# Optimization experiments

Hardware: AMD Instinct MI355X
Metric: run time of the kernel (lower is better)

## Reference

```python
import jax, jax.numpy as jnp
import numpy as np

B, C, H, W = 8, 128, 64, 64
INTER = C // 2

def setup_inputs() -> dict:
    key = jax.random.key(0)
    ks = jax.random.split(key, 9)
    s = 0.05
    return {
        "x": jax.random.normal(ks[0], (B, C, H, W), dtype=jnp.float32),
        "theta_w": jax.random.normal(ks[1], (INTER, C), dtype=jnp.float32) * s,
        "theta_b": jax.random.normal(ks[2], (INTER,), dtype=jnp.float32) * s,
        "phi_w": jax.random.normal(ks[3], (INTER, C), dtype=jnp.float32) * s,
        "phi_b": jax.random.normal(ks[4], (INTER,), dtype=jnp.float32) * s,
        "g_w": jax.random.normal(ks[5], (INTER, C), dtype=jnp.float32) * s,
        "g_b": jax.random.normal(ks[6], (INTER,), dtype=jnp.float32) * s,
        "out_w": jax.random.normal(ks[7], (C, INTER), dtype=jnp.float32) * s,
        "out_b": jax.random.normal(ks[8], (C,), dtype=jnp.float32) * s,
    }

def reference(x, theta_w, theta_b, phi_w, phi_b, g_w, g_b, out_w, out_b):
    b, c, h, w = x.shape
    xf = x.reshape(b, c, h * w)                                   # [b, C, n]
    # 1x1 convs == per-pixel channel matmuls
    theta = jnp.einsum('oc,bcn->bno', theta_w, xf) + theta_b       # [b, n, inter]
    phi = jnp.einsum('oc,bcn->bon', phi_w, xf) + phi_b[:, None]    # [b, inter, n]
    g = jnp.einsum('oc,bcn->bno', g_w, xf) + g_b                   # [b, n, inter]
    attn = jax.nn.softmax(jnp.einsum('bno,bom->bnm', theta, phi), axis=-1)  # [b, n, n]
    y = jnp.einsum('bnm,bmo->bon', attn, g)                        # [b, inter, n]
    out = jnp.einsum('oc,bcn->bon', out_w, y) + out_b[:, None]     # [b, C, n]
    return out.reshape(b, c, h, w) + x
```

## Files before the change

### kernel.cpp

```cpp
#include <hip/hip_runtime.h>
#include <hip/hip_bf16.h>
#include <cstdint>
#include <cmath>

#define N_PIX 4096
#define CH    128
#define DD    64
#define NBATCH 8
#define NT    32

typedef unsigned short u16;
typedef __attribute__((ext_vector_type(8))) short bf8_t;
typedef __attribute__((ext_vector_type(4))) float f4_t;
typedef __attribute__((ext_vector_type(16))) float f16v;
typedef uint32_t u32x4 __attribute__((ext_vector_type(4)));
typedef uint32_t u32x2 __attribute__((ext_vector_type(2)));

#define L2E 1.44269504088896340736f

#if __has_builtin(__builtin_amdgcn_exp2f)
  #define EXP2(x) __builtin_amdgcn_exp2f(x)
#else
  #define EXP2(x) exp2f(x)
#endif

__device__ __forceinline__ u16 f2b(float f) {
  union { float f; uint32_t u; } v; v.f = f;
  uint32_t u = v.u;
  return (u16)((u + 0x7fffu + ((u >> 16) & 1u)) >> 16);
}
__device__ __forceinline__ float b2f(u16 h) {
  union { uint32_t u; float f; } v; v.u = ((uint32_t)h) << 16;
  return v.f;
}
__device__ __forceinline__ uint32_t pack2(float a, float b) {
  return (uint32_t)f2b(a) | ((uint32_t)f2b(b) << 16);
}
__device__ __forceinline__ uint32_t pack2hw(float a, float b) {
  u16 lo = __builtin_bit_cast(u16, __float2bfloat16(a));
  u16 hi = __builtin_bit_cast(u16, __float2bfloat16(b));
  return (uint32_t)lo | ((uint32_t)hi << 16);
}
__device__ __forceinline__ f4_t mfma16(bf8_t a, bf8_t b, f4_t c) {
  return __builtin_amdgcn_mfma_f32_16x16x32_bf16(a, b, c, 0, 0, 0);
}
__device__ __forceinline__ f16v mfma32(bf8_t a, bf8_t b, f16v c) {
  return __builtin_amdgcn_mfma_f32_32x32x16_bf16(a, b, c, 0, 0, 0);
}
__device__ __forceinline__ void pl32swap(uint32_t &a, uint32_t &b) {
  u32x2 r = __builtin_amdgcn_permlane32_swap(a, b, false, false);
  a = r[0];
  b = r[1];
}

__global__ __launch_bounds__(256) void proj_kernel(
    const float* __restrict__ x,
    const float* __restrict__ tw, const float* __restrict__ tb,
    const float* __restrict__ pw, const float* __restrict__ pb,
    const float* __restrict__ gw, const float* __restrict__ gb,
    u16* __restrict__ theta_h, u16* __restrict__ phi_h, u16* __restrict__ gt_h) {
  __shared__ __align__(16) u16 xT[64][136];
  const int blk = blockIdx.x;
  const int b  = blk >> 6;
  const int n0 = (blk & 63) << 6;
  const int tid = threadIdx.x;

  #pragma unroll
  for (int i = 0; i < 8; ++i) {
    int idx = tid + i * 256;
    int px = (idx & 15) * 4;
    int c  = idx >> 4;
    float4 v = *(const float4*)(x + ((size_t)b * CH + c) * N_PIX + n0 + px);
    xT[px + 0][c] = f2b(v.x);
    xT[px + 1][c] = f2b(v.y);
    xT[px + 2][c] = f2b(v.z);
    xT[px + 3][c] = f2b(v.w);
  }
  __syncthreads();

  const int lane = tid & 63;
  const int w    = tid >> 6;
  const int l4   = lane >> 4, l15 = lane & 15;

  bf8_t bw[3][4];
  float bias[3];
  #pragma unroll
  for (int nt = 0; nt < 3; ++nt) {
    int op = 16 * (3 * w + nt) + l15;
    const float* wrow; float bv; float scl;
    if (op < 64)       { wrow = tw + op * CH;          bv = tb[op];        scl = L2E; }
    else if (op < 128) { wrow = pw + (op - 64) * CH;   bv = pb[op - 64];   scl = 1.f; }
    else               { wrow = gw + (op - 128) * CH;  bv = gb[op - 128];  scl = 1.f; }
    bias[nt] = bv * scl;
    #pragma unroll
    for (int ks = 0; ks < 4; ++ks) {
      const float* p = wrow + 32 * ks + l4 * 8;
      bf8_t v;
      #pragma unroll
      for (int j = 0; j < 8; ++j) v[j] = (short)f2b(p[j] * scl);
      bw[nt][ks] = v;
    }
  }

  f4_t acc[4][3];
  #pragma unroll
  for (int mt = 0; mt < 4; ++mt)
    #pragma unroll
    for (int nt = 0; nt < 3; ++nt) acc[mt][nt] = (f4_t){0.f, 0.f, 0.f, 0.f};

  #pragma unroll
  for (int mt = 0; mt < 4; ++mt) {
    #pragma unroll
    for (int ks = 0; ks < 4; ++ks) {
      bf8_t a = *(const bf8_t*)&xT[l15 + 16 * mt][32 * ks + l4 * 8];
      #pragma unroll
      for (int nt = 0; nt < 3; ++nt)
        acc[mt][nt] = mfma16(a, bw[nt][ks], acc[mt][nt]);
    }
  }

  #pragma unroll
  for (int nt = 0; nt < 3; ++nt) {
    int op = 16 * (3 * w + nt) + l15;
    #pragma unroll
    for (int mt = 0; mt < 4; ++mt) {
      #pragma unroll
      for (int r = 0; r < 4; ++r) {
        int q = n0 + 16 * mt + l4 * 4 + r;
        u16 h = f2b(acc[mt][nt][r] + bias[nt]);
        if (op < 64)       theta_h[((size_t)b * N_PIX + q) * DD + op] = h;
        else if (op < 128) phi_h[((size_t)b * N_PIX + q) * DD + (op - 64)] = h;
        else               gt_h[((size_t)b * DD + (op - 128)) * N_PIX + q] = h;
      }
    }
  }
}

__global__ __launch_bounds__(512, 4) void attn_kernel(
    const u16* __restrict__ theta_h, const u16* __restrict__ phi_h,
    const u16* __restrict__ gt_h, u16* __restrict__ y_h) {
  __shared__ __align__(16) u16 smem[32768];

  const int bid = blockIdx.x;
  const int lb  = (bid & 7) * 64 + (bid >> 3);
  const int b   = lb >> 6;
  const int q0  = (lb & 63) << 6;
  const int tid = threadIdx.x;
  const int l   = tid & 63;
  const int w   = tid >> 6;
  const int qg  = w & 1;
  const int mh  = w >> 1;
  const int l31 = l & 31;
  const int hi  = l >> 5;

  bf8_t th[4];
  {
    const u16* trow = theta_h + ((size_t)b * N_PIX + q0 + 32 * qg + l31) * DD;
    #pragma unroll
    for (int kk = 0; kk < 4; ++kk)
      th[kk] = *(const bf8_t*)(trow + 16 * kk + 8 * hi);
  }

  f16v yacc[2];
  #pragma unroll
  for (int ot = 0; ot < 2; ++ot)
    #pragma unroll
    for (int r = 0; r < 16; ++r) yacc[ot][r] = 0.f;
  float m_ = -1e30f, l_ = 0.f;

  const int pr  = tid >> 3, pc = tid & 7;
  const int go  = tid >> 4, gc = tid & 15;
  const u16* phA = phi_h + ((size_t)b * N_PIX + pr) * DD + pc * 8;
  const u16* gtA = gt_h + ((size_t)b * DD + go) * N_PIX + gc * 8;
  const int pO0 = pr * 64 + ((pc ^ (pr & 7)) << 3);
  const int pO1 = pO0 + 4096;
  const int gO0 = 8192 + go * 128 + ((gc ^ (go & 7)) << 3);
  const int gO1 = gO0 + 4096;

  uint4 v0, v1, v2, v3;
  #define LOADS(kb_) do {                                              \
    v0 = *(const uint4*)(phA + (size_t)(kb_) * 8192);                  \
    v1 = *(const uint4*)(phA + (size_t)(kb_) * 8192 + 4096);           \
    v2 = *(const uint4*)(gtA + (size_t)(kb_) * 128);                   \
    v3 = *(const uint4*)(gtA + (size_t)(kb_) * 128 + 32 * (size_t)N_PIX); \
  } while (0)
  #define WRITES(buf_) do {                                            \
    u16* base_ = smem + (buf_) * 16384;                                \
    *(uint4*)(base_ + pO0) = v0;                                       \
    *(uint4*)(base_ + pO1) = v1;                                       \
    *(uint4*)(base_ + gO0) = v2;                                       \
    *(uint4*)(base_ + gO1) = v3;                                       \
  } while (0)

  LOADS(0); WRITES(0);
  __syncthreads();

  const int prow  = 32 * mh + l31;
  const int pbase = prow * 64;
  const int pkey  = prow & 7;

  for (int t = 0; t < NT; ++t) {
    const int cur = t & 1;
    if (t < NT - 1) LOADS(t + 1);
    const u16* pb = smem + cur * 16384;
    const u16* gb = pb + 8192;

    f16v st;
    #pragma unroll
    for (int r = 0; r < 16; ++r) st[r] = 0.f;
    #pragma unroll
    for (int kk = 0; kk < 4; ++kk) {
      bf8_t a = *(const bf8_t*)(pb + pbase + (((2 * kk + hi) ^ pkey) << 3));
      st = mfma32(a, th[kk], st);
    }

    float x0 = fmaxf(st[0], st[1]),   x1 = fmaxf(st[2], st[3]);
    float x2 = fmaxf(st[4], st[5]),   x3 = fmaxf(st[6], st[7]);
    float x4 = fmaxf(st[8], st[9]),   x5 = fmaxf(st[10], st[11]);
    float x6 = fmaxf(st[12], st[13]), x7 = fmaxf(st[14], st[15]);
    float y0 = fmaxf(fmaxf(x0, x1), fmaxf(x2, x3));
    float y1 = fmaxf(fmaxf(x4, x5), fmaxf(x6, x7));
    float pmax = fmaxf(y0, y1);
    pmax = fmaxf(pmax, __shfl_xor(pmax, 32));

    if (!__all(pmax <= m_ + 8.f)) {
      float mn = fmaxf(m_, pmax);
      float sc = EXP2(m_ - mn);
      m_ = mn;
      l_ *= sc;
      #pragma unroll
      for (int ot = 0; ot < 2; ++ot)
        #pragma unroll
        for (int r = 0; r < 16; ++r) yacc[ot][r] *= sc;
    }

    #pragma unroll
    for (int r = 0; r < 16; ++r) st[r] = EXP2(st[r] - m_);
    float s0 = st[0] + st[1],   s1 = st[2] + st[3];
    float s2 = st[4] + st[5],   s3 = st[6] + st[7];
    float s4 = st[8] + st[9],   s5 = st[10] + st[11];
    float s6 = st[12] + st[13], s7 = st[14] + st[15];
    float t0 = (s0 + s1) + (s2 + s3);
    float t1 = (s4 + s5) + (s6 + s7);
    l_ += t0 + t1;

    uint32_t c0 = pack2hw(st[0],  st[1]),  c1 = pack2hw(st[2],  st[3]);
    uint32_t c2 = pack2hw(st[4],  st[5]),  c3 = pack2hw(st[6],  st[7]);
    uint32_t c4 = pack2hw(st[8],  st[9]),  c5 = pack2hw(st[10], st[11]);
    uint32_t c6 = pack2hw(st[12], st[13]), c7 = pack2hw(st[14], st[15]);
    pl32swap(c0, c2); pl32swap(c1, c3);
    pl32swap(c4, c6); pl32swap(c5, c7);
    bf8_t pf0 = __builtin_bit_cast(bf8_t, (u32x4){c0, c1, c2, c3});
    bf8_t pf1 = __builtin_bit_cast(bf8_t, (u32x4){c4, c5, c6, c7});

    #pragma unroll
    for (int ot = 0; ot < 2; ++ot) {
      int orow  = 32 * ot + l31;
      int obase = orow * 128;
      int okey  = orow & 7;
      bf8_t g0 = *(const bf8_t*)(gb + obase + ((((mh << 2) + hi)     ^ okey) << 3));
      yacc[ot] = mfma32(g0, pf0, yacc[ot]);
      bf8_t g1 = *(const bf8_t*)(gb + obase + ((((mh << 2) + 2 + hi) ^ okey) << 3));
      yacc[ot] = mfma32(g1, pf1, yacc[ot]);
    }

    if (t < NT - 1) WRITES(cur ^ 1);
    __syncthreads();
  }
  #undef LOADS
  #undef WRITES

  l_ += __shfl_xor(l_, 32);

  #pragma unroll
  for (int ot = 0; ot < 2; ++ot)
    #pragma unroll
    for (int r = 0; r < 16; ++r) {
      int o = 32 * ot + (r & 3) + 8 * (r >> 2) + 4 * hi;
      smem[(((qg * 4 + mh) * 64 + o) << 5) + l31] = f2b(yacc[ot][r]);
    }
  float* ml = (float*)(smem + 16384);
  if (hi == 0) {
    ml[(qg * 4 + mh) * 64 + l31]      = m_;
    ml[(qg * 4 + mh) * 64 + 32 + l31] = l_;
  }
  __syncthreads();

  {
    const int qg2 = tid >> 8;
    const int rem = tid & 255;
    const int qq  = rem & 31;
    const int og  = rem >> 5;
    float mi[4], li[4];
    #pragma unroll
    for (int i = 0; i < 4; ++i) {
      mi[i] = ml[(qg2 * 4 + i) * 64 + qq];
      li[i] = ml[(qg2 * 4 + i) * 64 + 32 + qq];
    }
    float M = fmaxf(fmaxf(mi[0], mi[1]), fmaxf(mi[2], mi[3]));
    float e[4], L = 0.f;
    #pragma unroll
    for (int i = 0; i < 4; ++i) { e[i] = EXP2(mi[i] - M); L += li[i] * e[i]; }
    float invL = 1.0f / L;
    float acc[8];
    #pragma unroll
    for (int oo = 0; oo < 8; ++oo) {
      int o = og * 8 + oo;
      float a = 0.f;
      #pragma unroll
      for (int i = 0; i < 4; ++i)
        a += b2f(smem[(((qg2 * 4 + i) * 64 + o) << 5) + qq]) * e[i];
      acc[oo] = a * invL;
    }
    uint4 ov;
    ov.x = pack2(acc[0], acc[1]);
    ov.y = pack2(acc[2], acc[3]);
    ov.z = pack2(acc[4], acc[5]);
    ov.w = pack2(acc[6], acc[7]);
    *(uint4*)(y_h + ((size_t)b * N_PIX + q0 + 32 * qg2 + qq) * DD + og * 8) = ov;
  }
}

__global__ __launch_bounds__(256) void outproj_kernel(
    const u16* __restrict__ y_h, const float* __restrict__ ow,
    const float* __restrict__ ob, const float* __restrict__ x,
    float* __restrict__ out) {
  __shared__ __align__(16) float ot[128][68];
  const int blk = blockIdx.x;
  const int b  = blk >> 6;
  const int n0 = (blk & 63) << 6;
  const int tid = threadIdx.x;
  const int lane = tid & 63;
  const int w    = tid >> 6;
  const int l4   = lane >> 4, l15 = lane & 15;

  bf8_t bw[2][2];
  float bias[2];
  #pragma unroll
  for (int nt = 0; nt < 2; ++nt) {
    int c = 16 * (2 * w + nt) + l15;
    bias[nt] = ob[c];
    #pragma unroll
    for (int ks = 0; ks < 2; ++ks) {
      const float* p = ow + c * DD + 32 * ks + l4 * 8;
      bf8_t v;
      #pragma unroll
      for (int j = 0; j < 8; ++j) v[j] = (short)f2b(p[j]);
      bw[nt][ks] = v;
    }
  }

  f4_t acc[4][2];
  #pragma unroll
  for (int mt = 0; mt < 4; ++mt)
    #pragma unroll
    for (int nt = 0; nt < 2; ++nt) acc[mt][nt] = (f4_t){0.f, 0.f, 0.f, 0.f};

  #pragma unroll
  for (int mt = 0; mt < 4; ++mt) {
    const u16* yr = y_h + ((size_t)b * N_PIX + n0 + 16 * mt + l15) * DD + l4 * 8;
    bf8_t a0 = *(const bf8_t*)yr;
    bf8_t a1 = *(const bf8_t*)(yr + 32);
    #pragma unroll
    for (int nt = 0; nt < 2; ++nt) {
      acc[mt][nt] = mfma16(a0, bw[nt][0], acc[mt][nt]);
      acc[mt][nt] = mfma16(a1, bw[nt][1], acc[mt][nt]);
    }
  }

  #pragma unroll
  for (int nt = 0; nt < 2; ++nt) {
    int c = 16 * (2 * w + nt) + l15;
    #pragma unroll
    for (int mt = 0; mt < 4; ++mt)
      #pragma unroll
      for (int r = 0; r < 4; ++r)
        ot[c][16 * mt + l4 * 4 + r] = acc[mt][nt][r] + bias[nt];
  }
  __syncthreads();

  #pragma unroll
  for (int i = 0; i < 8; ++i) {
    int idx = tid + i * 256;
    int px = (idx & 15) * 4;
    int c  = idx >> 4;
    size_t gi = ((size_t)b * CH + c) * N_PIX + n0 + px;
    float4 xv = *(const float4*)(x + gi);
    float4 o;
    o.x = ot[c][px + 0] + xv.x;
    o.y = ot[c][px + 1] + xv.y;
    o.z = ot[c][px + 2] + xv.z;
    o.w = ot[c][px + 3] + xv.w;
    *(float4*)(out + gi) = o;
  }
}

extern "C" void kernel_launch(void* const* d_in, const int* in_sizes, int n_in,
                              void* d_out, int out_size, void* d_ws, size_t ws_size,
                              hipStream_t stream) {
  const float* x  = (const float*)d_in[0];
  const float* tw = (const float*)d_in[1];
  const float* tb = (const float*)d_in[2];
  const float* pw = (const float*)d_in[3];
  const float* pb = (const float*)d_in[4];
  const float* gw = (const float*)d_in[5];
  const float* gb = (const float*)d_in[6];
  const float* ow = (const float*)d_in[7];
  const float* ob = (const float*)d_in[8];
  float* out = (float*)d_out;

  const size_t sz = (size_t)NBATCH * N_PIX * DD;
  u16* theta_h = (u16*)d_ws;
  u16* phi_h   = theta_h + sz;
  u16* gt_h    = phi_h + sz;
  u16* y_h     = gt_h + sz;

  proj_kernel<<<512, 256, 0, stream>>>(x, tw, tb, pw, pb, gw, gb, theta_h, phi_h, gt_h);
  attn_kernel<<<512, 512, 0, stream>>>(theta_h, phi_h, gt_h, y_h);
  outproj_kernel<<<512, 256, 0, stream>>>(y_h, ow, ob, x, out);
}
```

Before: 86.09 us.

## Load phi and g tiles directly from global into registers, drop LDS staging

Replaces the double-buffered shared-memory staging of phi and g^T tiles, and the per-iteration __syncthreads, with direct per-wave global loads into MFMA operand registers. Shared memory shrinks to what the epilogue needs, which may allow more resident blocks, and removes barrier stalls. The cost is that the two wave groups (qg) now both fetch the same phi/g data from global or L2, and load latency is no longer hidden by explicit prefetch.

New measurement: 146.7 us. 70.4% more time.

```diff
diff --git a/kernel.cpp b/kernel.cpp
--- a/kernel.cpp
+++ b/kernel.cpp
@@ -139,7 +139,7 @@
 __global__ __launch_bounds__(512, 4) void attn_kernel(
     const u16* __restrict__ theta_h, const u16* __restrict__ phi_h,
     const u16* __restrict__ gt_h, u16* __restrict__ y_h) {
-  __shared__ __align__(16) u16 smem[32768];
+  __shared__ __align__(16) u16 smem[17408];
 
   const int bid = blockIdx.x;
   const int lb  = (bid & 7) * 64 + (bid >> 3);
@@ -168,51 +168,30 @@
     for (int r = 0; r < 16; ++r) yacc[ot][r] = 0.f;
   float m_ = -1e30f, l_ = 0.f;
 
-  const int pr  = tid >> 3, pc = tid & 7;
-  const int go  = tid >> 4, gc = tid & 15;
-  const u16* phA = phi_h + ((size_t)b * N_PIX + pr) * DD + pc * 8;
-  const u16* gtA = gt_h + ((size_t)b * DD + go) * N_PIX + gc * 8;
-  const int pO0 = pr * 64 + ((pc ^ (pr & 7)) << 3);
-  const int pO1 = pO0 + 4096;
-  const int gO0 = 8192 + go * 128 + ((gc ^ (go & 7)) << 3);
-  const int gO1 = gO0 + 4096;
-
-  uint4 v0, v1, v2, v3;
-  #define LOADS(kb_) do {                                              \
-    v0 = *(const uint4*)(phA + (size_t)(kb_) * 8192);                  \
-    v1 = *(const uint4*)(phA + (size_t)(kb_) * 8192 + 4096);           \
-    v2 = *(const uint4*)(gtA + (size_t)(kb_) * 128);                   \
-    v3 = *(const uint4*)(gtA + (size_t)(kb_) * 128 + 32 * (size_t)N_PIX); \
-  } while (0)
-  #define WRITES(buf_) do {                                            \
-    u16* base_ = smem + (buf_) * 16384;                                \
-    *(uint4*)(base_ + pO0) = v0;                                       \
-    *(uint4*)(base_ + pO1) = v1;                                       \
-    *(uint4*)(base_ + gO0) = v2;                                       \
-    *(uint4*)(base_ + gO1) = v3;                                       \
-  } while (0)
-
-  LOADS(0); WRITES(0);
-  __syncthreads();
-
-  const int prow  = 32 * mh + l31;
-  const int pbase = prow * 64;
-  const int pkey  = prow & 7;
+  const u16* pP = phi_h + ((size_t)b * N_PIX + 32 * mh + l31) * DD + 8 * hi;
+  const u16* pG0 = gt_h + ((size_t)b * DD + l31) * N_PIX + mh * 32 + 8 * hi;
+  const u16* pG1 = pG0 + 32 * (size_t)N_PIX;
 
   for (int t = 0; t < NT; ++t) {
-    const int cur = t & 1;
-    if (t < NT - 1) LOADS(t + 1);
-    const u16* pb = smem + cur * 16384;
-    const u16* gb = pb + 8192;
+    bf8_t a0 = *(const bf8_t*)(pP);
+    bf8_t a1 = *(const bf8_t*)(pP + 16);
+    bf8_t a2 = *(const bf8_t*)(pP + 32);
+    bf8_t a3 = *(const bf8_t*)(pP + 48);
+    bf8_t g00 = *(const bf8_t*)(pG0);
+    bf8_t g01 = *(const bf8_t*)(pG0 + 16);
+    bf8_t g10 = *(const bf8_t*)(pG1);
+    bf8_t g11 = *(const bf8_t*)(pG1 + 16);
+    pP += 128 * DD;
+    pG0 += 128;
+    pG1 += 128;
 
     f16v st;
     #pragma unroll
     for (int r = 0; r < 16; ++r) st[r] = 0.f;
-    #pragma unroll
-    for (int kk = 0; kk < 4; ++kk) {
-      bf8_t a = *(const bf8_t*)(pb + pbase + (((2 * kk + hi) ^ pkey) << 3));
-      st = mfma32(a, th[kk], st);
-    }
+    st = mfma32(a0, th[0], st);
+    st = mfma32(a1, th[1], st);
+    st = mfma32(a2, th[2], st);
+    st = mfma32(a3, th[3], st);
 
     float x0 = fmaxf(st[0], st[1]),   x1 = fmaxf(st[2], st[3]);
     float x2 = fmaxf(st[4], st[5]),   x3 = fmaxf(st[6], st[7]);
@@ -253,22 +232,11 @@
     bf8_t pf0 = __builtin_bit_cast(bf8_t, (u32x4){c0, c1, c2, c3});
     bf8_t pf1 = __builtin_bit_cast(bf8_t, (u32x4){c4, c5, c6, c7});
 
-    #pragma unroll
-    for (int ot = 0; ot < 2; ++ot) {
-      int orow  = 32 * ot + l31;
-      int obase = orow * 128;
-      int okey  = orow & 7;
-      bf8_t g0 = *(const bf8_t*)(gb + obase + ((((mh << 2) + hi)     ^ okey) << 3));
-      yacc[ot] = mfma32(g0, pf0, yacc[ot]);
-      bf8_t g1 = *(const bf8_t*)(gb + obase + ((((mh << 2) + 2 + hi) ^ okey) << 3));
-      yacc[ot] = mfma32(g1, pf1, yacc[ot]);
-    }
-
-    if (t < NT - 1) WRITES(cur ^ 1);
-    __syncthreads();
-  }
-  #undef LOADS
-  #undef WRITES
+    yacc[0] = mfma32(g00, pf0, yacc[0]);
+    yacc[0] = mfma32(g01, pf1, yacc[0]);
+    yacc[1] = mfma32(g10, pf0, yacc[1]);
+    yacc[1] = mfma32(g11, pf1, yacc[1]);
+  }
 
   l_ += __shfl_xor(l_, 32);
 
```
